# Performance work log

Hardware: AMD Instinct MI355X
Metric: run time of the kernel (lower is better)

## Reference

```python
import jax, jax.numpy as jnp
import numpy as np

EPS = 1e-12  # matches torch F.normalize eps


def _l2_normalize(x):
    n = jnp.linalg.norm(x, axis=-1, keepdims=True)
    return x / jnp.maximum(n, EPS)


def setup_inputs() -> dict:
    key = jax.random.key(0)
    k1, k2, k3 = jax.random.split(key, 3)
    N, E, D = 100000, 1200000, 64
    feat = jax.random.normal(k1, (N, D), dtype=jnp.float32)
    beta = jnp.ones((1,), dtype=jnp.float32)
    src = jax.random.randint(k2, (E,), 0, N, dtype=jnp.int32)
    dst = jax.random.randint(k3, (E,), 0, N, dtype=jnp.int32)
    return {"feat": feat, "beta": beta, "src": src, "dst": dst}


def reference(feat, beta, src, dst):
    N = feat.shape[0]
    # cosine similarity on each edge (AGNN att_type)
    nh = _l2_normalize(feat)                                  # [N, D]
    e = beta[0] * jnp.sum(nh[src] * nh[dst], axis=-1)         # [E]
    # edge softmax over incoming edges of each destination node
    emax = jax.ops.segment_max(e, dst, num_segments=N)        # [N]
    emax = jnp.where(jnp.isfinite(emax), emax, 0.0)           # isolated nodes
    p = jnp.exp(e - emax[dst])                                # [E]
    psum = jax.ops.segment_sum(p, dst, num_segments=N)        # [N]
    p = p / jnp.maximum(psum[dst], EPS)                       # [E]
    # weighted scatter-sum aggregation: h_i' = sum_j p_ij * h_j
    msg = feat[src] * p[:, None]                              # [E, D]
    out = jax.ops.segment_sum(msg, dst, num_segments=N)       # [N, D]
    return out
```

## Files before the change

kernel.cpp:

```cpp
#include <hip/hip_runtime.h>
#include <hip/hip_fp16.h>

#define D 64
#define EPS 1e-12f
#define NPB 512
#define NPB_SHIFT 9
#define NB 256
#define CAP 8192
#define CAP_SHIFT 13
#define EPB 4096
#define SRC_BITS 17

typedef _Float16 hv2 __attribute__((ext_vector_type(2)));

__device__ inline unsigned bc_u(__half2 h) { return __builtin_bit_cast(unsigned, h); }
__device__ inline __half2  bc_h(unsigned u) { return __builtin_bit_cast(__half2, u); }

__device__ inline float fdot2f(unsigned a, unsigned b, float c) {
#if defined(__has_builtin) && __has_builtin(__builtin_amdgcn_fdot2)
    return __builtin_amdgcn_fdot2(__builtin_bit_cast(hv2, a),
                                  __builtin_bit_cast(hv2, b), c, false);
#else
    __half2 ah = bc_h(a), bh = bc_h(b);
    return c + __low2float(ah) * __low2float(bh)
             + __high2float(ah) * __high2float(bh);
#endif
}

__global__ __launch_bounds__(512) void scatter_kernel(
        const int* __restrict__ src,
        const int* __restrict__ dst,
        int* __restrict__ bincursor,
        unsigned* __restrict__ pairs, int E) {
    __shared__ int hist[NB], gbase[NB];
    int tid  = threadIdx.x;
    int base = blockIdx.x * EPB;
    int cnt  = min(EPB, E - base);

    if (tid < NB) hist[tid] = 0;
    __syncthreads();

    unsigned rec[8];
    int      meta[8];
    #pragma unroll
    for (int k = 0; k < 8; k++) {
        int i = tid + (k << 9);
        if (i < cnt) {
            int s = src[base + i], dd = dst[base + i];
            int b = dd >> NPB_SHIFT;
            rec[k]  = ((unsigned)(dd & (NPB - 1)) << SRC_BITS) | (unsigned)s;
            meta[k] = (b << 16) | atomicAdd(&hist[b], 1);
        } else meta[k] = -1;
    }
    __syncthreads();
    if (tid < NB) {
        int v = hist[tid];
        if (v > 0)
            gbase[tid] = (tid << CAP_SHIFT) + atomicAdd(&bincursor[tid], v);
    }
    __syncthreads();
    #pragma unroll
    for (int k = 0; k < 8; k++)
        if (meta[k] >= 0)
            pairs[gbase[meta[k] >> 16] + (meta[k] & 0xffff)] = rec[k];
}

__global__ __launch_bounds__(1024) void csr_nh_kernel(
        const unsigned* __restrict__ pairs,
        const int* __restrict__ bincursor,
        int* __restrict__ rowbeg,
        int* __restrict__ rowend,
        int* __restrict__ esrc,
        const float4* __restrict__ feat4,
        float* __restrict__ norms,
        uint2* __restrict__ nh2,
        int N, int nbins) {
    __shared__ int hist[NPB], offs[NPB];
    __shared__ int wsum[8];

    if ((int)blockIdx.x >= nbins) {
        int gid = (blockIdx.x - nbins) * 1024 + threadIdx.x;
        int row = gid >> 4;
        int lg  = gid & 15;
        if (row >= N) return;
        float4 v = feat4[row * 16 + lg];
        float ss = v.x * v.x + v.y * v.y + v.z * v.z + v.w * v.w;
        #pragma unroll
        for (int off = 1; off < 16; off <<= 1) ss += __shfl_xor(ss, off, 64);
        float nrm = fmaxf(sqrtf(ss), EPS);
        float inv = 1.0f / nrm;
        if (lg == 0) norms[row] = nrm;
        uint2 p;
        p.x = bc_u(__floats2half2_rn(v.x * inv, v.y * inv));
        p.y = bc_u(__floats2half2_rn(v.z * inv, v.w * inv));
        nh2[row * 16 + lg] = p;
        return;
    }

    int b    = blockIdx.x;
    int tid  = threadIdx.x;
    int base = b << CAP_SHIFT;
    int cnt  = bincursor[b];
    int node0 = b << NPB_SHIFT;

    if (tid < NPB) hist[tid] = 0;
    __syncthreads();

    unsigned rec[8];
    int      meta[8];
    #pragma unroll
    for (int k = 0; k < 8; k++) {
        int i = tid + (k << 10);
        if (i < cnt) {
            unsigned p = pairs[base + i];
            int ln  = (int)(p >> SRC_BITS);
            rec[k]  = p & ((1u << SRC_BITS) - 1);
            meta[k] = (ln << 16) | atomicAdd(&hist[ln], 1);
        } else meta[k] = -1;
    }
    __syncthreads();
    int lane = tid & 63, w = tid >> 6;
    int v = 0, x = 0;
    if (tid < NPB) { v = hist[tid]; x = v; }
    #pragma unroll
    for (int off = 1; off < 64; off <<= 1) {
        int t = __shfl_up(x, off, 64);
        if (lane >= off) x += t;
    }
    if (tid < NPB && lane == 63) wsum[w] = x;
    __syncthreads();
    if (tid < NPB) {
        int add = 0;
        #pragma unroll
        for (int ww = 0; ww < 8; ww++) add += (ww < w) ? wsum[ww] : 0;
        int excl = x + add - v;
        offs[tid] = excl;
        int node = node0 + tid;
        if (node < N) { rowbeg[node] = base + excl; rowend[node] = base + excl + v; }
    }
    __syncthreads();
    #pragma unroll
    for (int k = 0; k < 8; k++)
        if (meta[k] >= 0)
            esrc[base + offs[meta[k] >> 16] + (meta[k] & 0xffff)] = (int)rec[k];
}

__global__ __launch_bounds__(256) void gather_kernel(const uint4* __restrict__ nh4,
                                                     const float* __restrict__ norms,
                                                     const float* __restrict__ beta_p,
                                                     const int* __restrict__ rowbeg,
                                                     const int* __restrict__ rowend,
                                                     const int* __restrict__ esrc,
                                                     float4* __restrict__ out4, int N) {
    int t    = blockIdx.x * 256 + threadIdx.x;
    int lane = threadIdx.x & 63;
    int g    = lane >> 3;
    int lg   = lane & 7;
    int d    = (t >> 6) * 8 + g;
    if (d >= N) return;

    int j   = rowbeg[d];
    int end = rowend[d];
    float beta = beta_p[0];

    uint4 fdp = nh4[(size_t)d * 8 + lg];

    __half2 acc0 = __float2half2_rn(0.f), acc1 = acc0, acc2 = acc0, acc3 = acc0;
    float ps = 0.f;

    for (; j < end; j += 4) {
        bool v1 = (j + 1 < end), v2 = (j + 2 < end), v3 = (j + 3 < end);
        int s0 = esrc[j];
        int s1 = v1 ? esrc[j + 1] : s0;
        int s2 = v2 ? esrc[j + 2] : s0;
        int s3 = v3 ? esrc[j + 3] : s0;
        uint4 p0 = nh4[(size_t)s0 * 8 + lg];
        uint4 p1 = nh4[(size_t)s1 * 8 + lg];
        uint4 p2 = nh4[(size_t)s2 * 8 + lg];
        uint4 p3 = nh4[(size_t)s3 * 8 + lg];
        float n0 = norms[s0], n1 = norms[s1], n2 = norms[s2], n3 = norms[s3];
        float d0 = fdot2f(p0.x, fdp.x, 0.f), d1 = fdot2f(p1.x, fdp.x, 0.f);
        float d2 = fdot2f(p2.x, fdp.x, 0.f), d3 = fdot2f(p3.x, fdp.x, 0.f);
        d0 = fdot2f(p0.y, fdp.y, d0); d1 = fdot2f(p1.y, fdp.y, d1);
        d2 = fdot2f(p2.y, fdp.y, d2); d3 = fdot2f(p3.y, fdp.y, d3);
        d0 = fdot2f(p0.z, fdp.z, d0); d1 = fdot2f(p1.z, fdp.z, d1);
        d2 = fdot2f(p2.z, fdp.z, d2); d3 = fdot2f(p3.z, fdp.z, d3);
        d0 = fdot2f(p0.w, fdp.w, d0); d1 = fdot2f(p1.w, fdp.w, d1);
        d2 = fdot2f(p2.w, fdp.w, d2); d3 = fdot2f(p3.w, fdp.w, d3);
        #pragma unroll
        for (int off = 1; off < 8; off <<= 1) {
            d0 += __shfl_xor(d0, off, 64);
            d1 += __shfl_xor(d1, off, 64);
            d2 += __shfl_xor(d2, off, 64);
            d3 += __shfl_xor(d3, off, 64);
        }
        float w0 = __expf(beta * d0);
        float w1 = v1 ? __expf(beta * d1) : 0.f;
        float w2 = v2 ? __expf(beta * d2) : 0.f;
        float w3 = v3 ? __expf(beta * d3) : 0.f;
        __half2 q0 = __float2half2_rn(w0 * n0);
        __half2 q1 = __float2half2_rn(w1 * n1);
        __half2 q2 = __float2half2_rn(w2 * n2);
        __half2 q3 = __float2half2_rn(w3 * n3);
        acc0 = __hfma2(q0, bc_h(p0.x), acc0); acc0 = __hfma2(q1, bc_h(p1.x), acc0);
        acc0 = __hfma2(q2, bc_h(p2.x), acc0); acc0 = __hfma2(q3, bc_h(p3.x), acc0);
        acc1 = __hfma2(q0, bc_h(p0.y), acc1); acc1 = __hfma2(q1, bc_h(p1.y), acc1);
        acc1 = __hfma2(q2, bc_h(p2.y), acc1); acc1 = __hfma2(q3, bc_h(p3.y), acc1);
        acc2 = __hfma2(q0, bc_h(p0.z), acc2); acc2 = __hfma2(q1, bc_h(p1.z), acc2);
        acc2 = __hfma2(q2, bc_h(p2.z), acc2); acc2 = __hfma2(q3, bc_h(p3.z), acc2);
        acc3 = __hfma2(q0, bc_h(p0.w), acc3); acc3 = __hfma2(q1, bc_h(p1.w), acc3);
        acc3 = __hfma2(q2, bc_h(p2.w), acc3); acc3 = __hfma2(q3, bc_h(p3.w), acc3);
        ps += w0 + w1 + w2 + w3;
    }

    float r = 1.0f / fmaxf(ps, EPS);
    float4 o0 = {__low2float(acc0) * r, __high2float(acc0) * r,
                 __low2float(acc1) * r, __high2float(acc1) * r};
    float4 o1 = {__low2float(acc2) * r, __high2float(acc2) * r,
                 __low2float(acc3) * r, __high2float(acc3) * r};
    out4[(size_t)d * 16 + lg * 2]     = o0;
    out4[(size_t)d * 16 + lg * 2 + 1] = o1;
}

extern "C" void kernel_launch(void* const* d_in, const int* in_sizes, int n_in,
                              void* d_out, int out_size, void* d_ws, size_t ws_size,
                              hipStream_t stream) {
    const float* feat = (const float*)d_in[0];
    const float* beta = (const float*)d_in[1];
    const int*   src  = (const int*)d_in[2];
    const int*   dst  = (const int*)d_in[3];

    int N = in_sizes[0] / D;
    int E = in_sizes[2];
    int nbins = (N + NPB - 1) / NPB;

    unsigned* pairs     = (unsigned*)d_ws;
    int*      esrc      = (int*)(pairs + (size_t)nbins * CAP);
    unsigned* nhraw     = (unsigned*)(esrc + (size_t)nbins * CAP);
    float*    norms     = (float*)(nhraw + (size_t)N * 32);
    int*      bincursor = (int*)(norms + N);
    int*      rowbeg    = bincursor + NB;
    int*      rowend    = rowbeg + N;

    hipMemsetAsync(bincursor, 0, NB * sizeof(int), stream);

    int BS = (E + EPB - 1) / EPB;
    int BI = (N * 16 + 1023) / 1024;
    scatter_kernel<<<BS, 512, 0, stream>>>(src, dst, bincursor, pairs, E);
    csr_nh_kernel<<<nbins + BI, 1024, 0, stream>>>(
        pairs, bincursor, rowbeg, rowend, esrc,
        (const float4*)feat, norms, (uint2*)nhraw, N, nbins);
    gather_kernel<<<(N + 31) / 32, 256, 0, stream>>>(
        (const uint4*)nhraw, norms, beta, rowbeg, rowend, esrc,
        (float4*)d_out, N);
}
```

Baseline: 137.5 us.

## Replace global-atomic bin scatter with per-block local sort and fragment gather

The scatter kernel now sorts each 4096-edge chunk by destination bin in shared memory and writes the chunk contiguously, together with per-block bin offsets. This replaces scattered global writes and global atomics on the bin cursors. The CSR kernel then pulls each bin's fragments from all chunk blocks into shared memory using a prefix scan over fragment lengths. This gives coalesced writes and drops the memset, but adds a second shared-memory pass, an offset table of about 293x257 entries, and many short, poorly coalesced fragment reads (about 18 edges each) in the CSR stage.

```diff
diff --git a/kernel.cpp b/kernel.cpp
--- a/kernel.cpp
+++ b/kernel.cpp
@@ -9,6 +9,7 @@
 #define CAP 8192
 #define CAP_SHIFT 13
 #define EPB 4096
+#define FRAG_MAX 512
 #define SRC_BITS 17
 
 typedef _Float16 hv2 __attribute__((ext_vector_type(2)));
@@ -27,56 +28,75 @@
 #endif
 }
 
-__global__ __launch_bounds__(512) void scatter_kernel(
+__global__ __launch_bounds__(1024) void scatter_kernel(
         const int* __restrict__ src,
         const int* __restrict__ dst,
-        int* __restrict__ bincursor,
+        int* __restrict__ offs_g,
         unsigned* __restrict__ pairs, int E) {
-    __shared__ int hist[NB], gbase[NB];
+    __shared__ int hist[NB], offs[NB + 1], cursor[NB];
+    __shared__ int wsum[4];
+    __shared__ int dstbuf[EPB];
+    __shared__ unsigned buf[EPB];
+
     int tid  = threadIdx.x;
     int base = blockIdx.x * EPB;
     int cnt  = min(EPB, E - base);
 
     if (tid < NB) hist[tid] = 0;
     __syncthreads();
-
-    unsigned rec[8];
-    int      meta[8];
+    for (int i = tid; i < cnt; i += 1024) {
+        int dd = dst[base + i];
+        dstbuf[i] = dd;
+        atomicAdd(&hist[dd >> NPB_SHIFT], 1);
+    }
+    __syncthreads();
+    int lane = tid & 63, w = tid >> 6;
+    int v = 0, x = 0;
+    if (tid < NB) { v = hist[tid]; x = v; }
     #pragma unroll
-    for (int k = 0; k < 8; k++) {
-        int i = tid + (k << 9);
-        if (i < cnt) {
-            int s = src[base + i], dd = dst[base + i];
-            int b = dd >> NPB_SHIFT;
-            rec[k]  = ((unsigned)(dd & (NPB - 1)) << SRC_BITS) | (unsigned)s;
-            meta[k] = (b << 16) | atomicAdd(&hist[b], 1);
-        } else meta[k] = -1;
-    }
+    for (int off = 1; off < 64; off <<= 1) {
+        int t = __shfl_up(x, off, 64);
+        if (lane >= off) x += t;
+    }
+    if (tid < NB && lane == 63) wsum[w] = x;
     __syncthreads();
     if (tid < NB) {
-        int v = hist[tid];
-        if (v > 0)
-            gbase[tid] = (tid << CAP_SHIFT) + atomicAdd(&bincursor[tid], v);
-    }
-    __syncthreads();
-    #pragma unroll
-    for (int k = 0; k < 8; k++)
-        if (meta[k] >= 0)
-            pairs[gbase[meta[k] >> 16] + (meta[k] & 0xffff)] = rec[k];
+        int add = 0;
+        #pragma unroll
+        for (int ww = 0; ww < 4; ww++) add += (ww < w) ? wsum[ww] : 0;
+        int excl = x + add - v;
+        offs[tid] = excl; cursor[tid] = excl;
+    }
+    if (tid == 0) offs[NB] = cnt;
+    __syncthreads();
+    for (int i = tid; i < cnt; i += 1024) {
+        int s = src[base + i], dd = dstbuf[i];
+        int b = dd >> NPB_SHIFT;
+        int l = atomicAdd(&cursor[b], 1);
+        buf[l] = ((unsigned)(dd & (NPB - 1)) << SRC_BITS) | (unsigned)s;
+    }
+    __syncthreads();
+    for (int i = tid; i < cnt; i += 1024)
+        pairs[base + i] = buf[i];
+    for (int i = tid; i <= NB; i += 1024)
+        offs_g[blockIdx.x * (NB + 1) + i] = offs[i];
 }
 
 __global__ __launch_bounds__(1024) void csr_nh_kernel(
         const unsigned* __restrict__ pairs,
-        const int* __restrict__ bincursor,
+        const int* __restrict__ offs_g,
         int* __restrict__ rowbeg,
         int* __restrict__ rowend,
         int* __restrict__ esrc,
         const float4* __restrict__ feat4,
         float* __restrict__ norms,
         uint2* __restrict__ nh2,
-        int N, int nbins) {
-    __shared__ int hist[NPB], offs[NPB];
+        int N, int nbins, int nblk) {
+    __shared__ unsigned buf[CAP];
+    __shared__ int fragsrc[FRAG_MAX], fraglen[FRAG_MAX], fragdst[FRAG_MAX];
+    __shared__ int hist[NPB], offsL[NPB];
     __shared__ int wsum[8];
+    __shared__ int totcnt;
 
     if ((int)blockIdx.x >= nbins) {
         int gid = (blockIdx.x - nbins) * 1024 + threadIdx.x;
@@ -99,27 +119,57 @@
 
     int b    = blockIdx.x;
     int tid  = threadIdx.x;
+    int lane = tid & 63, w = tid >> 6;
     int base = b << CAP_SHIFT;
-    int cnt  = bincursor[b];
     int node0 = b << NPB_SHIFT;
 
+    for (int f = tid; f < nblk; f += 1024) {
+        int o0 = offs_g[f * (NB + 1) + b];
+        int o1 = offs_g[f * (NB + 1) + b + 1];
+        fragsrc[f] = o0;
+        fraglen[f] = o1 - o0;
+    }
+    __syncthreads();
+    if (tid < 64) {
+        int carry = 0;
+        for (int c = 0; c < nblk; c += 64) {
+            int idx = c + tid;
+            int ld = (idx < nblk) ? fraglen[idx] : 0;
+            int x = ld;
+            #pragma unroll
+            for (int off = 1; off < 64; off <<= 1) {
+                int t = __shfl_up(x, off, 64);
+                if (tid >= off) x += t;
+            }
+            if (idx < nblk) fragdst[idx] = carry + x - ld;
+            carry += __shfl(x, 63, 64);
+        }
+        if (tid == 0) totcnt = carry;
+    }
     if (tid < NPB) hist[tid] = 0;
     __syncthreads();
-
+    for (int f = w; f < nblk; f += 16) {
+        int len = fraglen[f];
+        int sb = f * EPB + fragsrc[f];
+        int db = fragdst[f];
+        for (int j = lane; j < len; j += 64)
+            buf[db + j] = pairs[sb + j];
+    }
+    __syncthreads();
+    int cnt = totcnt;
     unsigned rec[8];
     int      meta[8];
     #pragma unroll
     for (int k = 0; k < 8; k++) {
         int i = tid + (k << 10);
         if (i < cnt) {
-            unsigned p = pairs[base + i];
+            unsigned p = buf[i];
             int ln  = (int)(p >> SRC_BITS);
             rec[k]  = p & ((1u << SRC_BITS) - 1);
             meta[k] = (ln << 16) | atomicAdd(&hist[ln], 1);
         } else meta[k] = -1;
     }
     __syncthreads();
-    int lane = tid & 63, w = tid >> 6;
     int v = 0, x = 0;
     if (tid < NPB) { v = hist[tid]; x = v; }
     #pragma unroll
@@ -134,7 +184,7 @@
         #pragma unroll
         for (int ww = 0; ww < 8; ww++) add += (ww < w) ? wsum[ww] : 0;
         int excl = x + add - v;
-        offs[tid] = excl;
+        offsL[tid] = excl;
         int node = node0 + tid;
         if (node < N) { rowbeg[node] = base + excl; rowend[node] = base + excl + v; }
     }
@@ -142,7 +192,7 @@
     #pragma unroll
     for (int k = 0; k < 8; k++)
         if (meta[k] >= 0)
-            esrc[base + offs[meta[k] >> 16] + (meta[k] & 0xffff)] = (int)rec[k];
+            esrc[base + offsL[meta[k] >> 16] + (meta[k] & 0xffff)] = (int)rec[k];
 }
 
 __global__ __launch_bounds__(256) void gather_kernel(const uint4* __restrict__ nh4,
@@ -233,23 +283,21 @@
     int N = in_sizes[0] / D;
     int E = in_sizes[2];
     int nbins = (N + NPB - 1) / NPB;
-
-    unsigned* pairs     = (unsigned*)d_ws;
-    int*      esrc      = (int*)(pairs + (size_t)nbins * CAP);
-    unsigned* nhraw     = (unsigned*)(esrc + (size_t)nbins * CAP);
-    float*    norms     = (float*)(nhraw + (size_t)N * 32);
-    int*      bincursor = (int*)(norms + N);
-    int*      rowbeg    = bincursor + NB;
-    int*      rowend    = rowbeg + N;
-
-    hipMemsetAsync(bincursor, 0, NB * sizeof(int), stream);
-
-    int BS = (E + EPB - 1) / EPB;
+    int nblk  = (E + EPB - 1) / EPB;
+
+    unsigned* pairs  = (unsigned*)d_ws;
+    int*      esrc   = (int*)(pairs + (size_t)nblk * EPB);
+    int*      offs_g = esrc + (size_t)nbins * CAP;
+    unsigned* nhraw  = (unsigned*)(offs_g + (size_t)nblk * (NB + 1));
+    float*    norms  = (float*)(nhraw + (size_t)N * 32);
+    int*      rowbeg = (int*)(norms + N);
+    int*      rowend = rowbeg + N;
+
     int BI = (N * 16 + 1023) / 1024;
-    scatter_kernel<<<BS, 512, 0, stream>>>(src, dst, bincursor, pairs, E);
+    scatter_kernel<<<nblk, 1024, 0, stream>>>(src, dst, offs_g, pairs, E);
     csr_nh_kernel<<<nbins + BI, 1024, 0, stream>>>(
-        pairs, bincursor, rowbeg, rowend, esrc,
-        (const float4*)feat, norms, (uint2*)nhraw, N, nbins);
+        pairs, offs_g, rowbeg, rowend, esrc,
+        (const float4*)feat, norms, (uint2*)nhraw, N, nbins, nblk);
     gather_kernel<<<(N + 31) / 32, 256, 0, stream>>>(
         (const uint4*)nhraw, norms, beta, rowbeg, rowend, esrc,
         (float4*)d_out, N);
```

Measured after the change: 147.6 us. +7.4%, slower.
